# Kernel tuning notes

Measured on AMD Instinct MI355X. Metric: run time of the kernel, lower is better.

The kernel has to match this reference:

```python
import jax, jax.numpy as jnp
import numpy as np

CONF_THRES = 0.25
IOU_THRES = 0.45
MAX_WH = 7680.0   # class-separation offset (class-aware NMS trick)
K = 1024          # max candidates entering NMS per image
MAX_DET = 300     # max detections returned per image


def _pairwise_iou(boxes):
    # boxes: [K,4] xyxy -> iou: [K,K]
    x1, y1, x2, y2 = boxes[:, 0], boxes[:, 1], boxes[:, 2], boxes[:, 3]
    area = (x2 - x1) * (y2 - y1)
    ix1 = jnp.maximum(x1[:, None], x1[None, :])
    iy1 = jnp.maximum(y1[:, None], y1[None, :])
    ix2 = jnp.minimum(x2[:, None], x2[None, :])
    iy2 = jnp.minimum(y2[:, None], y2[None, :])
    inter = jnp.clip(ix2 - ix1, 0.0) * jnp.clip(iy2 - iy1, 0.0)
    union = area[:, None] + area[None, :] - inter
    return inter / (union + 1e-9)


def _nms_single(pred):
    # pred: [N, 5+nc]
    xywh = pred[:, :4]
    obj = pred[:, 4]
    cls_conf = obj[:, None] * pred[:, 5:]            # [N, nc]
    score = cls_conf.max(axis=-1)                    # best-class confidence
    cls_id = cls_conf.argmax(axis=-1)                # best class

    # confidence filter (masked, fixed shape): invalid -> score sentinel -1
    masked = jnp.where(score > CONF_THRES, score, -1.0)
    top_s, top_i = jax.lax.top_k(masked, K)          # sorted descending
    keep0 = top_s > CONF_THRES                       # valid candidates

    b = xywh[top_i]                                  # [K,4]
    sc = score[top_i]
    c = cls_id[top_i].astype(pred.dtype)

    # xywh -> xyxy
    cx, cy, w, h = b[:, 0], b[:, 1], b[:, 2], b[:, 3]
    boxes = jnp.stack([cx - w / 2, cy - h / 2, cx + w / 2, cy + h / 2], axis=-1)

    # class-aware NMS: offset boxes by class index so classes never overlap
    off_boxes = boxes + (c * MAX_WH)[:, None]
    iou = _pairwise_iou(off_boxes)                   # [K,K]

    idx = jnp.arange(K)
    def body(i, keep):
        # if box i is kept, suppress all later boxes with IoU > thresh
        sup = (iou[i] > IOU_THRES) & keep[i] & (idx > i)
        return keep & ~sup
    keep = jax.lax.fori_loop(0, K, body, keep0)

    # select top MAX_DET kept detections (scores already descending)
    order = jnp.argsort(-jnp.where(keep, top_s, -1.0))[:MAX_DET]
    det = jnp.concatenate([boxes, sc[:, None], c[:, None]], axis=-1)  # [K,6]
    out = jnp.where(keep[order][:, None], det[order], 0.0)            # [MAX_DET,6]
    return out


def setup_inputs() -> dict:
    key = jax.random.key(0)
    x = jax.random.uniform(key, (16, 25200, 85), dtype=jnp.float32)
    return {"x": x}


def reference(x):
    # x: [B, N, 5+nc] raw predictions (sigmoid-activated)
    # returns [B, MAX_DET, 6] = (x1, y1, x2, y2, conf, cls), zero-padded
    return jax.vmap(_nms_single)(x)
```

## Files before the change

### kernel.cpp

```cpp
#include <hip/hip_runtime.h>
#include <hip/hip_bf16.h>
#include <stdint.h>


#define NB 16
#define NA 25200
#define NK 1024
#define ND 300
#define CAP 2048
#define NBIN 4096

__device__ __forceinline__ uint32_t fkey(float f) {
    uint32_t b = __float_as_uint(f);
    return (b & 0x80000000u) ? ~b : (b | 0x80000000u);
}

__device__ __forceinline__ int score_bin(float s) {
    float f = (s - 0.25f) * (4096.0f / 0.75f);
    int b = (int)f;
    return b > (NBIN - 1) ? (NBIN - 1) : (b < 0 ? 0 : b);
}

__device__ __forceinline__ float key_score(uint32_t u) {
    uint32_t fb = (u & 0x80000000u) ? (u ^ 0x80000000u) : ~u;
    return __uint_as_float(fb);
}

__global__ void score_kernel(const float* __restrict__ x,
                             float4* __restrict__ boxes,
                             unsigned long long* __restrict__ candw) {
    int b = blockIdx.y;
    int a = blockIdx.x * 16 + (threadIdx.x >> 4);
    int lane = threadIdx.x & 15;
    const float* p = x + (size_t)(b * NA + a) * 85;
    float obj = p[4];
    float best = -1e30f;
    int bi = 0;
#pragma unroll
    for (int r = 0; r < 5; ++r) {
        int j = lane + 16 * r;
        float v = obj * p[5 + j];
        if (v > best) { best = v; bi = j; }
    }
    for (int off = 8; off >= 1; off >>= 1) {
        float ov = __shfl_xor(best, off, 16);
        int   oi = __shfl_xor(bi,   off, 16);
        if (ov > best || (ov == best && oi < bi)) { best = ov; bi = oi; }
    }
    if (lane == 0) {
        float cx = p[0], cy = p[1], w = p[2], h = p[3];
        boxes[b * NA + a] = make_float4(cx - w * 0.5f, cy - h * 0.5f,
                                        cx + w * 0.5f, cy + h * 0.5f);
        unsigned long long key = 0ULL;
        if (best > 0.25f)
            key = ((unsigned long long)fkey(best) << 32) |
                  ((unsigned long long)(unsigned)(NA - 1 - a) << 7) |
                  (unsigned)bi;
        candw[(size_t)b * NA + a] = key;
    }
}

__global__ void __launch_bounds__(1024)
select_sort_kernel(const unsigned long long* __restrict__ candw,
                   const float4* __restrict__ boxes,
                   float4* __restrict__ obox,
                   float* __restrict__ det,
                   unsigned long long* __restrict__ keep0w) {
    int b = blockIdx.x;
    int t = threadIdx.x;
    int wid = t >> 6, lane = t & 63;
    __shared__ unsigned int lhist[NBIN];
    __shared__ unsigned long long sk[CAP];
    __shared__ unsigned int wsum[16];
    __shared__ int sB;
    __shared__ unsigned int scnt;

    const ulonglong2* cb2 = (const ulonglong2*)(candw + (size_t)b * NA);

    ((uint4*)lhist)[t] = make_uint4(0u, 0u, 0u, 0u);
    sk[t] = 0ULL; sk[t + 1024] = 0ULL;
    if (t == 0) { sB = -1; scnt = 0u; }
    __syncthreads();
    for (int i = t; i < NA / 2; i += 1024) {
        ulonglong2 k2 = cb2[i];
        if (k2.x)
            atomicAdd(&lhist[score_bin(key_score((uint32_t)(k2.x >> 32)))], 1u);
        if (k2.y)
            atomicAdd(&lhist[score_bin(key_score((uint32_t)(k2.y >> 32)))], 1u);
    }
    __syncthreads();

    uint4 hv = ((const uint4*)lhist)[t];
    unsigned int mysum = hv.x + hv.y + hv.z + hv.w;
    unsigned int ssfx = mysum;
#pragma unroll
    for (int off = 1; off < 64; off <<= 1) {
        unsigned int v = __shfl_down(ssfx, off);
        if (lane + off < 64) ssfx += v;
    }
    if (lane == 0) wsum[wid] = ssfx;
    __syncthreads();
    unsigned int tail = 0;
    for (int w2 = wid + 1; w2 < 16; ++w2) tail += wsum[w2];
    unsigned int S_t = ssfx + tail;
    unsigned int Snext = S_t - mysum;
    unsigned int s3 = hv.w + Snext;
    unsigned int s2 = hv.z + s3;
    unsigned int s1 = hv.y + s2;
    unsigned int s0 = hv.x + s1;
    int loc = -1;
    if (s3 >= NK) loc = t * 4 + 3;
    else if (s2 >= NK) loc = t * 4 + 2;
    else if (s1 >= NK) loc = t * 4 + 1;
    else if (s0 >= NK) loc = t * 4 + 0;
#pragma unroll
    for (int off = 32; off >= 1; off >>= 1) {
        int o = __shfl_xor(loc, off);
        loc = o > loc ? o : loc;
    }
    if ((t & 63) == 0) atomicMax(&sB, loc);
    __syncthreads();
    int B = sB < 0 ? 0 : sB;

    for (int i = t; i < NA / 2; i += 1024) {
        ulonglong2 k2 = cb2[i];
        unsigned long long ke[2] = {k2.x, k2.y};
#pragma unroll
        for (int e = 0; e < 2; ++e) {
            unsigned long long k = ke[e];
            bool q = (k != 0ULL) &&
                     (score_bin(key_score((uint32_t)(k >> 32))) >= B);
            unsigned long long m = __ballot(q);
            if (q) {
                int nbelow = __popcll(m & ((1ULL << lane) - 1));
                int leader = __ffsll((long long)m) - 1;
                unsigned int base = 0;
                if (lane == leader)
                    base = atomicAdd(&scnt, (unsigned int)__popcll(m));
                base = __shfl(base, leader);
                unsigned int pos = base + nbelow;
                if (pos < CAP) sk[pos] = k;
            }
        }
    }
    __syncthreads();

    const int e1 = t, e2 = t + 1024;
    unsigned long long v1 = sk[e1];
    unsigned long long v2 = sk[e2];
    __syncthreads();
    for (int k = 2; k <= CAP; k <<= 1) {
        for (int j = k >> 1; j > 0; j >>= 1) {
            if (j >= 1024) {
                unsigned long long lo = v1 < v2 ? v1 : v2;
                unsigned long long hi = v1 < v2 ? v2 : v1;
                v1 = hi; v2 = lo;
            } else if (j >= 64) {
                sk[e1] = v1; sk[e2] = v2;
                __syncthreads();
                unsigned long long p1 = sk[e1 ^ j], p2 = sk[e2 ^ j];
                __syncthreads();
                {
                    bool takeMax = (((e1 & j) == 0) == ((e1 & k) == 0));
                    bool g = p1 > v1;
                    v1 = (takeMax == g) ? p1 : v1;
                }
                {
                    bool takeMax = (((e2 & j) == 0) == ((e2 & k) == 0));
                    bool g = p2 > v2;
                    v2 = (takeMax == g) ? p2 : v2;
                }
            } else {
                {
                    unsigned long long p1 =
                        (unsigned long long)__shfl_xor((long long)v1, j);
                    bool takeMax = (((e1 & j) == 0) == ((e1 & k) == 0));
                    bool g = p1 > v1;
                    v1 = (takeMax == g) ? p1 : v1;
                }
                {
                    unsigned long long p2 =
                        (unsigned long long)__shfl_xor((long long)v2, j);
                    bool takeMax = (((e2 & j) == 0) == ((e2 & k) == 0));
                    bool g = p2 > v2;
                    v2 = (takeMax == g) ? p2 : v2;
                }
            }
        }
    }
    unsigned long long key = v1;
    uint32_t u = (uint32_t)(key >> 32);
    uint32_t low = (uint32_t)key;
    int a = (u == 0) ? 0 : (int)(NA - 1 - (low >> 7));
    int cls = (u == 0) ? 0 : (int)(low & 0x7Fu);
    float s = key_score(u);
    float4 bx = boxes[b * NA + a];
    float c = (float)cls;
    float off = c * 7680.0f;
    obox[b * NK + t] =
        make_float4(bx.x + off, bx.y + off, bx.z + off, bx.w + off);
    float* dr = det + (size_t)(b * NK + t) * 8;
    dr[0] = bx.x; dr[1] = bx.y; dr[2] = bx.z; dr[3] = bx.w;
    dr[4] = s; dr[5] = c;
    bool keep0 = s > 0.25f;
    unsigned long long bal = __ballot(keep0);
    if ((t & 63) == 0) keep0w[b * 16 + (t >> 6)] = bal;
}

__global__ void mask_kernel(const float4* __restrict__ obox,
                            unsigned long long* __restrict__ maskm) {
    int cb = blockIdx.x, rb = blockIdx.y, b = blockIdx.z;
    if (cb > rb) return;
    int t = threadIdx.x;
    int i = rb * 64 + t;
    __shared__ float4 cbox[64];
    __shared__ float carea[64];
    int j0 = cb * 64;
    float4 c4 = obox[b * NK + j0 + t];
    cbox[t] = c4;
    carea[t] = (c4.z - c4.x) * (c4.w - c4.y);
    __syncthreads();
    float4 r4 = obox[b * NK + i];
    float ra = (r4.z - r4.x) * (r4.w - r4.y);
    unsigned long long word = 0;
    for (int jj = 0; jj < 64; ++jj) {
        int j = j0 + jj;
        float4 o = cbox[jj];
        if (j < i && fabsf(r4.x - o.x) < 3840.0f) {
            float ix1 = fmaxf(r4.x, o.x), iy1 = fmaxf(r4.y, o.y);
            float ix2 = fminf(r4.z, o.z), iy2 = fminf(r4.w, o.w);
            float iw = fmaxf(ix2 - ix1, 0.0f), ih = fmaxf(iy2 - iy1, 0.0f);
            float inter = iw * ih;
            float uni = ra + carea[jj] - inter;
            float iou = inter / (uni + 1e-9f);
            if (iou > 0.45f) word |= (1ULL << jj);
        }
    }
    maskm[(size_t)(b * 16 + cb) * NK + i] = word;
}

__global__ void __launch_bounds__(1024)
jacobi_out_kernel(const unsigned long long* __restrict__ maskm,
                  const unsigned long long* __restrict__ keep0w,
                  const float* __restrict__ det,
                  float* __restrict__ out) {
    int b = blockIdx.x;
    int t = threadIdx.x;
    int wid = t >> 6, lane = t & 63;
    __shared__ unsigned long long aliveS[16];
    __shared__ int changedS;
    __shared__ int list[ND];
    __shared__ int totalS;

    unsigned long long row[16];
#pragma unroll
    for (int w = 0; w < 16; ++w)
        row[w] = (w <= wid) ? maskm[(size_t)(b * 16 + w) * NK + t] : 0ULL;
    bool keep0 = (keep0w[b * 16 + wid] >> lane) & 1ULL;
    if (t < 16) aliveS[t] = keep0w[b * 16 + t];
    __syncthreads();

    for (int it = 0; it < NK; ++it) {
        if (t == 0) changedS = 0;
        unsigned long long aw[16];
#pragma unroll
        for (int w = 0; w < 16; ++w) aw[w] = aliveS[w];
        __syncthreads();
        unsigned long long sup = 0;
#pragma unroll
        for (int w = 0; w < 16; ++w) sup |= aw[w] & row[w];
        bool newalive = keep0 && (sup == 0);
        unsigned long long nb = __ballot(newalive);
        if (lane == 0) {
            if (nb != aw[wid]) { atomicOr(&changedS, 1); aliveS[wid] = nb; }
        }
        __syncthreads();
        if (!changedS) break;
    }

    if (t < 64) {
        unsigned long long av = (lane < 16) ? aliveS[lane] : 0ULL;
        int cnt2 = (lane < 16) ? __popcll(av) : 0;
        int pre = cnt2;
        for (int off = 1; off < 64; off <<= 1) {
            int v = __shfl_up(pre, off);
            if (lane >= off) pre += v;
        }
        int total = __shfl(pre, 63);
        int base = pre - cnt2;
        if (lane == 0) totalS = total;
        if (lane < 16) {
            unsigned long long m = av;
            int pos = base;
            while (m && pos < ND) {
                int bit = __ffsll((long long)m) - 1;
                list[pos++] = lane * 64 + bit;
                m &= m - 1;
            }
        }
    }
    __syncthreads();
    if (t < ND) {
        float vals[6] = {0, 0, 0, 0, 0, 0};
        if (t < totalS) {
            const float* dr = det + (size_t)(b * NK + list[t]) * 8;
#pragma unroll
            for (int c = 0; c < 6; ++c) vals[c] = dr[c];
        }
        float* o = out + (size_t)(b * ND + t) * 6;
#pragma unroll
        for (int c = 0; c < 6; ++c) o[c] = vals[c];
    }
}

extern "C" void kernel_launch(void* const* d_in, const int* in_sizes, int n_in,
                              void* d_out, int out_size, void* d_ws, size_t ws_size,
                              hipStream_t stream) {
    const float* x = (const float*)d_in[0];
    float* out = (float*)d_out;

    char* ws = (char*)d_ws;
    size_t off = 0;
    auto alloc = [&](size_t bytes) {
        void* p = ws + off;
        off += (bytes + 255) & ~(size_t)255;
        return p;
    };
    float4* boxes = (float4*)alloc((size_t)NB * NA * sizeof(float4));
    unsigned long long* candw =
        (unsigned long long*)alloc((size_t)NB * NA * sizeof(unsigned long long));
    float4* obox = (float4*)alloc((size_t)NB * NK * sizeof(float4));
    float* det = (float*)alloc((size_t)NB * NK * 8 * sizeof(float));
    unsigned long long* keep0w =
        (unsigned long long*)alloc((size_t)NB * 16 * sizeof(unsigned long long));
    unsigned long long* maskm =
        (unsigned long long*)alloc((size_t)NB * NK * 16 * sizeof(unsigned long long));
    (void)ws_size;

    score_kernel<<<dim3(NA / 16, NB), 256, 0, stream>>>(x, boxes, candw);
    select_sort_kernel<<<NB, 1024, 0, stream>>>(candw, boxes, obox, det,
                                                keep0w);
    mask_kernel<<<dim3(16, 16, NB), 64, 0, stream>>>(obox, maskm);
    jacobi_out_kernel<<<NB, 1024, 0, stream>>>(maskm, keep0w, det, out);
}
```

Before: 85.63 us.

## Fuse IoU mask build into NMS kernel using per-class candidate bitmasks

Removes the separate mask kernel and its global suppression-matrix round trip. Boxes are staged in shared memory inside the per-image NMS kernel. Each thread computes IoU only against earlier candidates of the same class, found through per-class bitmasks built with shared atomics. This saves one launch and the global traffic, and skips cross-class pairs. In exchange, only 16 blocks do the IoU work, and warps may diverge unevenly when class counts differ.

```diff
diff --git a/kernel.cpp b/kernel.cpp
--- a/kernel.cpp
+++ b/kernel.cpp
@@ -9,6 +9,7 @@
 #define ND 300
 #define CAP 2048
 #define NBIN 4096
+#define NCLS 80
 
 __device__ __forceinline__ uint32_t fkey(float f) {
     uint32_t b = __float_as_uint(f);
@@ -207,57 +208,59 @@
     if ((t & 63) == 0) keep0w[b * 16 + (t >> 6)] = bal;
 }
 
-__global__ void mask_kernel(const float4* __restrict__ obox,
-                            unsigned long long* __restrict__ maskm) {
-    int cb = blockIdx.x, rb = blockIdx.y, b = blockIdx.z;
-    if (cb > rb) return;
-    int t = threadIdx.x;
-    int i = rb * 64 + t;
-    __shared__ float4 cbox[64];
-    __shared__ float carea[64];
-    int j0 = cb * 64;
-    float4 c4 = obox[b * NK + j0 + t];
-    cbox[t] = c4;
-    carea[t] = (c4.z - c4.x) * (c4.w - c4.y);
-    __syncthreads();
-    float4 r4 = obox[b * NK + i];
-    float ra = (r4.z - r4.x) * (r4.w - r4.y);
-    unsigned long long word = 0;
-    for (int jj = 0; jj < 64; ++jj) {
-        int j = j0 + jj;
-        float4 o = cbox[jj];
-        if (j < i && fabsf(r4.x - o.x) < 3840.0f) {
-            float ix1 = fmaxf(r4.x, o.x), iy1 = fmaxf(r4.y, o.y);
-            float ix2 = fminf(r4.z, o.z), iy2 = fminf(r4.w, o.w);
-            float iw = fmaxf(ix2 - ix1, 0.0f), ih = fmaxf(iy2 - iy1, 0.0f);
-            float inter = iw * ih;
-            float uni = ra + carea[jj] - inter;
-            float iou = inter / (uni + 1e-9f);
-            if (iou > 0.45f) word |= (1ULL << jj);
-        }
-    }
-    maskm[(size_t)(b * 16 + cb) * NK + i] = word;
-}
-
 __global__ void __launch_bounds__(1024)
-jacobi_out_kernel(const unsigned long long* __restrict__ maskm,
-                  const unsigned long long* __restrict__ keep0w,
-                  const float* __restrict__ det,
-                  float* __restrict__ out) {
+nms_out_kernel(const float4* __restrict__ obox,
+               const float* __restrict__ det,
+               const unsigned long long* __restrict__ keep0w,
+               float* __restrict__ out) {
     int b = blockIdx.x;
     int t = threadIdx.x;
     int wid = t >> 6, lane = t & 63;
+    __shared__ float4 oboxS[NK];
+    __shared__ unsigned long long cmaskS[NCLS * 16];
     __shared__ unsigned long long aliveS[16];
     __shared__ int changedS;
     __shared__ int list[ND];
     __shared__ int totalS;
 
-    unsigned long long row[16];
-#pragma unroll
-    for (int w = 0; w < 16; ++w)
-        row[w] = (w <= wid) ? maskm[(size_t)(b * 16 + w) * NK + t] : 0ULL;
+    float4 ob = obox[b * NK + t];
+    const float* dr = det + (size_t)(b * NK + t) * 8;
+    float s = dr[4];
+    int ci = (int)dr[5];
+    oboxS[t] = ob;
+    cmaskS[t] = 0ULL;
+    if (t < NCLS * 16 - 1024) cmaskS[1024 + t] = 0ULL;
     bool keep0 = (keep0w[b * 16 + wid] >> lane) & 1ULL;
     if (t < 16) aliveS[t] = keep0w[b * 16 + t];
+    __syncthreads();
+    atomicOr(&cmaskS[ci * 16 + wid], 1ULL << lane);
+    (void)s;
+    __syncthreads();
+
+    unsigned long long row[16];
+#pragma unroll
+    for (int w = 0; w < 16; ++w) row[w] = 0ULL;
+    float ra = (ob.z - ob.x) * (ob.w - ob.y);
+    for (int w = 0; w <= wid; ++w) {
+        unsigned long long bits = cmaskS[ci * 16 + w];
+        if (w == wid)
+            bits &= (lane == 0) ? 0ULL : ((1ULL << lane) - 1ULL);
+        unsigned long long rbits = 0ULL;
+        while (bits) {
+            int bit = __ffsll((long long)bits) - 1;
+            bits &= bits - 1;
+            float4 o = oboxS[w * 64 + bit];
+            float carea = (o.z - o.x) * (o.w - o.y);
+            float ix1 = fmaxf(ob.x, o.x), iy1 = fmaxf(ob.y, o.y);
+            float ix2 = fminf(ob.z, o.z), iy2 = fminf(ob.w, o.w);
+            float iw = fmaxf(ix2 - ix1, 0.0f), ih = fmaxf(iy2 - iy1, 0.0f);
+            float inter = iw * ih;
+            float uni = ra + carea - inter;
+            float iou = inter / (uni + 1e-9f);
+            if (iou > 0.45f) rbits |= (1ULL << bit);
+        }
+        row[w] = rbits;
+    }
     __syncthreads();
 
     for (int it = 0; it < NK; ++it) {
@@ -303,9 +306,9 @@
     if (t < ND) {
         float vals[6] = {0, 0, 0, 0, 0, 0};
         if (t < totalS) {
-            const float* dr = det + (size_t)(b * NK + list[t]) * 8;
-#pragma unroll
-            for (int c = 0; c < 6; ++c) vals[c] = dr[c];
+            const float* dr2 = det + (size_t)(b * NK + list[t]) * 8;
+#pragma unroll
+            for (int c = 0; c < 6; ++c) vals[c] = dr2[c];
         }
         float* o = out + (size_t)(b * ND + t) * 6;
 #pragma unroll
@@ -333,13 +336,10 @@
     float* det = (float*)alloc((size_t)NB * NK * 8 * sizeof(float));
     unsigned long long* keep0w =
         (unsigned long long*)alloc((size_t)NB * 16 * sizeof(unsigned long long));
-    unsigned long long* maskm =
-        (unsigned long long*)alloc((size_t)NB * NK * 16 * sizeof(unsigned long long));
     (void)ws_size;
 
     score_kernel<<<dim3(NA / 16, NB), 256, 0, stream>>>(x, boxes, candw);
     select_sort_kernel<<<NB, 1024, 0, stream>>>(candw, boxes, obox, det,
                                                 keep0w);
-    mask_kernel<<<dim3(16, 16, NB), 64, 0, stream>>>(obox, maskm);
-    jacobi_out_kernel<<<NB, 1024, 0, stream>>>(maskm, keep0w, det, out);
-}
+    nms_out_kernel<<<NB, 1024, 0, stream>>>(obox, det, keep0w, out);
+}
```

After: 82.99 us. -3.1%, faster.
